# Kernel tuning notes

Hardware: AMD Instinct MI355X
Metric: run time of the kernel (lower is better)

Reference implementation:

```python
import jax, jax.numpy as jnp
import numpy as np

H = 1024      # hidden_dim
NH = 16       # num_heads
HD = H // NH  # head_dim
EPS = 1e-12
SCALE = float(np.sqrt(H))


def setup_inputs() -> dict:
    key = jax.random.key(0)
    ks = jax.random.split(key, 12)
    S, B = 2048, 2
    inp = {
        "query": jax.random.normal(ks[0], (S, B, 2 * H), jnp.float32),
        "key":   jax.random.normal(ks[1], (S, B, H), jnp.float32),
        "value": jax.random.normal(ks[2], (S, B, H), jnp.float32),
        # gating params (zeros in torch init, but randomize for a meaningful test)
        "qs": jax.random.normal(ks[3], (1, 1, H), jnp.float32) * 0.02,
        "ks_p": jax.random.normal(ks[4], (1, 1, H), jnp.float32) * 0.02,
        "vs": jax.random.normal(ks[5], (1, 1, H), jnp.float32) * 0.02,
        # Overparam vq: Linear(H, 2H)
        "vq_w": jax.random.normal(ks[6], (2 * H, H), jnp.float32) * (1.0 / np.sqrt(H)),
        "vq_b": jax.random.normal(ks[7], (2 * H,), jnp.float32) * 0.02,
        # q_linear: Linear(2H, H)
        "ql_w": jax.random.normal(ks[8], (H, 2 * H), jnp.float32) * (1.0 / np.sqrt(2 * H)),
        "ql_b": jax.random.normal(ks[9], (H,), jnp.float32) * 0.02,
        # LayerNorm(H)
        "ln_g": jnp.ones((H,), jnp.float32),
        "ln_b": jnp.zeros((H,), jnp.float32),
    }
    return inp


def _layernorm(x, g, b):
    mu = jnp.mean(x, axis=-1, keepdims=True)
    var = jnp.mean(jnp.square(x - mu), axis=-1, keepdims=True)
    return (x - mu) * jax.lax.rsqrt(var + EPS) * g + b


def reference(query, key, value, qs, ks_p, vs, vq_w, vq_b, ql_w, ql_b, ln_g, ln_b):
    # gate vectors
    qsig = jax.nn.sigmoid(qs)            # [1,1,H]
    ksig = jax.nn.sigmoid(ks_p)          # [1,1,H]
    # vq = Overparam(sigmoid(vs)): c,f = l1(x).split(H); sigmoid(f)*tanh(c)
    h = jax.nn.sigmoid(vs) @ vq_w.T + vq_b   # [1,1,2H]
    c, f = h[..., :H], h[..., H:]
    vsig = jax.nn.sigmoid(f) * jnp.tanh(c)   # [1,1,H]

    q = qsig * _layernorm(query @ ql_w.T + ql_b, ln_g, ln_b)  # [S,B,H]
    k = ksig * key
    v = vsig * value

    # batch-first
    q = jnp.transpose(q, (1, 0, 2))  # [B,Q,H]
    k = jnp.transpose(k, (1, 0, 2))  # [B,K,H]
    v = jnp.transpose(v, (1, 0, 2))
    B, Q, _ = q.shape
    K = k.shape[1]

    qh = q.reshape(B, Q, NH, HD)
    kh = k.reshape(B, K, NH, HD)
    vh = v.reshape(B, K, NH, HD)

    scores = jnp.einsum('bqhd,bkhd->bhqk', qh, kh) / SCALE
    w = jax.nn.softmax(scores, axis=-1)                # [B,NH,Q,K]
    out = jnp.einsum('bhqk,bkhd->bqhd', w, vh).reshape(B, Q, H)
    # torch code's final .transpose(0,1) is not assigned -> output is [Q,B,H]
    return jnp.transpose(out, (1, 0, 2))
```

## Files before the change

### kernel.cpp

```cpp
#include <hip/hip_runtime.h>

typedef __bf16 bf16x8 __attribute__((ext_vector_type(8)));
typedef float f32x4 __attribute__((ext_vector_type(4)));
typedef unsigned short u16x8 __attribute__((ext_vector_type(8)));
typedef unsigned short u16x4 __attribute__((ext_vector_type(4)));
typedef unsigned short u16;
typedef unsigned int u32;


#define LOG2E 1.4426950408889634f

__device__ __forceinline__ float b2f(u16 u) {
  union { unsigned int i; float f; } x; x.i = ((unsigned int)u) << 16; return x.f;
}
__device__ __forceinline__ u16 f2b(float f) {
  union { float f; unsigned int i; } x; x.f = f;
  unsigned int r = (x.i + 0x7fffu + ((x.i >> 16) & 1u)) >> 16;
  return (u16)r;
}
__device__ __forceinline__ float sigm(float x) { return 1.0f / (1.0f + __expf(-x)); }

__device__ __forceinline__ void async16(u16* lds, const u16* g) {
  __builtin_amdgcn_global_load_lds((const __attribute__((address_space(1))) void*)g,
                                   (__attribute__((address_space(3))) void*)lds, 16, 0, 0);
}

__global__ __launch_bounds__(256) void k_cvt_all(const float4* __restrict__ q, u16x4* __restrict__ qd,
                                                 const float4* __restrict__ w, u16x4* __restrict__ wd,
                                                 const float4* __restrict__ k, u16x4* __restrict__ kd,
                                                 const float4* __restrict__ v, u16x4* __restrict__ vd) {
  int b = blockIdx.x;
  const float4* s; u16x4* d; int i;
  if (b < 8192)       { s = q; d = qd; i = b * 256 + threadIdx.x; }
  else if (b < 10240) { s = w; d = wd; i = (b - 8192) * 256 + threadIdx.x; }
  else if (b < 14336) { s = k; d = kd; i = (b - 10240) * 256 + threadIdx.x; }
  else                { s = v; d = vd; i = (b - 14336) * 256 + threadIdx.x; }
  float4 x = s[i];
  u16x4 o; o[0] = f2b(x.x); o[1] = f2b(x.y); o[2] = f2b(x.z); o[3] = f2b(x.w);
  d[i] = o;
}

__global__ __launch_bounds__(256) void k_h(const float* __restrict__ vs,
                                           const float* __restrict__ vq_w,
                                           const float* __restrict__ vq_b,
                                           float* __restrict__ h) {
  __shared__ float svs[1024];
  int t = threadIdx.x;
  for (int i = t; i < 1024; i += 256) svs[i] = sigm(vs[i]);
  __syncthreads();
  int wave = t >> 6, lane = t & 63;
  int row = blockIdx.x * 4 + wave;
  const float4* w4 = (const float4*)(vq_w + (size_t)row * 1024);
  const float4* s4 = (const float4*)svs;
  float acc = 0.f;
#pragma unroll
  for (int k = 0; k < 4; ++k) {
    float4 w = w4[k * 64 + lane];
    float4 s = s4[k * 64 + lane];
    acc += w.x * s.x + w.y * s.y + w.z * s.z + w.w * s.w;
  }
#pragma unroll
  for (int off = 1; off < 64; off <<= 1) acc += __shfl_xor(acc, off);
  if (lane == 0) h[row] = acc + vq_b[row];
}

__global__ __launch_bounds__(256) void k_gemm(const u16* __restrict__ A,
                                              const u16* __restrict__ Bt,
                                              u16* __restrict__ C) {
  __shared__ __align__(16) u16 As[128 * 32];
  __shared__ __align__(16) u16 Bs[128 * 32];
  int tid = threadIdx.x;
  int wave = tid >> 6, lane = tid & 63;
  int l15 = lane & 15, quad = lane >> 4;
  int bx = blockIdx.x & 255;
  int kh = blockIdx.x >> 8;
  int kofs = kh << 10;
  int m0 = (bx >> 3) * 128;
  int n0 = (bx & 7) * 128;
  int wm = (wave >> 1) * 64, wn = (wave & 1) * 64;
  f32x4 acc[4][4] = {};
  int c1 = tid, c2 = tid + 256;
  const u16* ga1 = A + (size_t)(m0 + (c1 >> 2)) * 2048 + kofs + (c1 & 3) * 8;
  const u16* ga2 = A + (size_t)(m0 + (c2 >> 2)) * 2048 + kofs + (c2 & 3) * 8;
  const u16* gb1 = Bt + (size_t)(n0 + (c1 >> 2)) * 2048 + kofs + (c1 & 3) * 8;
  const u16* gb2 = Bt + (size_t)(n0 + (c2 >> 2)) * 2048 + kofs + (c2 & 3) * 8;
  u16* lA1 = As + wave * 512;
  u16* lA2 = As + 2048 + wave * 512;
  u16* lB1 = Bs + wave * 512;
  u16* lB2 = Bs + 2048 + wave * 512;
  for (int kt = 0; kt < 32; ++kt) {
    async16(lA1, ga1); async16(lA2, ga2);
    async16(lB1, gb1); async16(lB2, gb2);
    ga1 += 32; ga2 += 32; gb1 += 32; gb2 += 32;
    __syncthreads();
    bf16x8 af[4], bfr[4];
#pragma unroll
    for (int mt = 0; mt < 4; ++mt)
      af[mt] = *(const bf16x8*)(As + (wm + mt * 16 + l15) * 32 + quad * 8);
#pragma unroll
    for (int nt = 0; nt < 4; ++nt)
      bfr[nt] = *(const bf16x8*)(Bs + (wn + nt * 16 + l15) * 32 + quad * 8);
#pragma unroll
    for (int mt = 0; mt < 4; ++mt)
#pragma unroll
      for (int nt = 0; nt < 4; ++nt)
        acc[mt][nt] = __builtin_amdgcn_mfma_f32_16x16x32_bf16(af[mt], bfr[nt], acc[mt][nt], 0, 0, 0);
    __syncthreads();
  }
  u16* Cp = C + (size_t)kh * 4096 * 1024;
#pragma unroll
  for (int mt = 0; mt < 4; ++mt) {
#pragma unroll
    for (int r = 0; r < 4; ++r) {
      int m = m0 + wm + mt * 16 + quad * 4 + r;
      u16* crow = Cp + (size_t)m * 1024 + n0 + wn + l15;
#pragma unroll
      for (int nt = 0; nt < 4; ++nt) crow[nt * 16] = f2b(acc[mt][nt][r]);
    }
  }
}

__global__ __launch_bounds__(256) void k_ln(const u16* __restrict__ qpre0,
                                            const u16* __restrict__ qpre1,
                                            const float* __restrict__ ql_b,
                                            const float* __restrict__ ln_g,
                                            const float* __restrict__ ln_b,
                                            const float* __restrict__ qs,
                                            const float* __restrict__ ks,
                                            u16* __restrict__ qatt) {
  int row = blockIdx.x;
  int t = threadIdx.x;
  u16x4 a4 = *(const u16x4*)(qpre0 + (size_t)row * 1024 + t * 4);
  u16x4 b4 = *(const u16x4*)(qpre1 + (size_t)row * 1024 + t * 4);
  float v[4];
  float s = 0.f, ss = 0.f;
#pragma unroll
  for (int j = 0; j < 4; ++j) {
    v[j] = b2f(a4[j]) + b2f(b4[j]) + ql_b[t * 4 + j];
    s += v[j]; ss += v[j] * v[j];
  }
#pragma unroll
  for (int off = 1; off < 64; off <<= 1) { s += __shfl_xor(s, off); ss += __shfl_xor(ss, off); }
  __shared__ float red[8];
  int wv = t >> 6, ln = t & 63;
  if (ln == 0) { red[wv] = s; red[4 + wv] = ss; }
  __syncthreads();
  s = red[0] + red[1] + red[2] + red[3];
  ss = red[4] + red[5] + red[6] + red[7];
  float mu = s * (1.f / 1024.f);
  float rstd = rsqrtf(ss * (1.f / 1024.f) - mu * mu + 1e-12f);
  int sidx = row >> 1, b = row & 1;
  int ch0 = t * 4;
  int hh = ch0 >> 6, hd0 = ch0 & 63;
  u16* dst = qatt + ((size_t)(b * 16 + hh) * 2048 + sidx) * 64 + hd0;
#pragma unroll
  for (int j = 0; j < 4; ++j) {
    int ch = ch0 + j;
    float gate = sigm(qs[ch]) * sigm(ks[ch]) * (LOG2E / 32.0f);
    float y = (v[j] - mu) * rstd * ln_g[ch] + ln_b[ch];
    dst[j] = f2b(y * gate);
  }
}

__global__ __launch_bounds__(256, 2) void k_attn(const u16* __restrict__ qatt,
                                                 const u16* __restrict__ key,
                                                 const u16* __restrict__ value,
                                                 const float* __restrict__ hbuf,
                                                 float* __restrict__ out) {
  int bh = blockIdx.x & 31;
  int qt = blockIdx.x >> 5;
  int b = bh >> 4, h = bh & 15;
  int tid = threadIdx.x, wave = tid >> 6, lane = tid & 63;
  int l15 = lane & 15, quad = lane >> 4;
  int q0 = qt * 128;

  __shared__ __align__(16) u16 Kt[2][64 * 72];
  __shared__ __align__(16) u16 Vt[2][64 * 72];
  __shared__ __align__(16) u16 Pb[4][32 * 72];

  bf16x8 qf[2][2];
#pragma unroll
  for (int f = 0; f < 2; ++f) {
    const u16* qrow = qatt + ((size_t)bh * 2048 + q0 + f * 64 + wave * 16 + l15) * 64 + quad * 8;
    qf[f][0] = *(const bf16x8*)qrow;
    qf[f][1] = *(const bf16x8*)(qrow + 32);
  }

  const u16* kb = key + (size_t)b * 1024 + (size_t)h * 64;
  const u16* vb = value + (size_t)b * 1024 + (size_t)h * 64;
  u16* Pw = Pb[wave];

  int p = lane & 31;
  int chbase = wave * 16 + (lane >> 5) * 8;
  const u16* vsrc = vb + (size_t)2 * p * 2048 + chbase;
  int krow = wave * 16 + (lane >> 3);
  int kch  = (lane & 7) * 8;
  const u16* ksrc = kb + (size_t)krow * 2048 + kch;
  int kdofs = krow * 72 + kch;
  int vdofs_base = 2 * p;

  {
    u16x8 k0 = *(const u16x8*)ksrc;
    u16x8 k1 = *(const u16x8*)(ksrc + (size_t)8 * 2048);
    *(u16x8*)(&Kt[0][kdofs]) = k0;
    *(u16x8*)(&Kt[0][kdofs + 8 * 72]) = k1;
    u16x8 va = *(const u16x8*)vsrc;
    u16x8 vbq = *(const u16x8*)(vsrc + 2048);
#pragma unroll
    for (int c = 0; c < 8; ++c) {
      u32 pk = (u32)va[c] | ((u32)vbq[c] << 16);
      *(u32*)(&Vt[0][(chbase + c) * 72 + vdofs_base]) = pk;
    }
  }
  __syncthreads();

  f32x4 oacc[2][4] = {};
  float l_i[2][4] = {};

  for (int kt = 0; kt < 32; ++kt) {
    int cur = kt & 1;
    f32x4 sacc[2][4] = {};
    const u16* ktc = Kt[cur];
#pragma unroll
    for (int nt = 0; nt < 4; ++nt) {
      const u16* kr = ktc + (nt * 16 + l15) * 72 + quad * 8;
      bf16x8 kfa = *(const bf16x8*)kr;
      bf16x8 kfb = *(const bf16x8*)(kr + 32);
      sacc[0][nt] = __builtin_amdgcn_mfma_f32_16x16x32_bf16(qf[0][0], kfa, sacc[0][nt], 0, 0, 0);
      sacc[0][nt] = __builtin_amdgcn_mfma_f32_16x16x32_bf16(qf[0][1], kfb, sacc[0][nt], 0, 0, 0);
      sacc[1][nt] = __builtin_amdgcn_mfma_f32_16x16x32_bf16(qf[1][0], kfa, sacc[1][nt], 0, 0, 0);
      sacc[1][nt] = __builtin_amdgcn_mfma_f32_16x16x32_bf16(qf[1][1], kfb, sacc[1][nt], 0, 0, 0);
    }
    u16x8 pk0, pk1, va, vbq;
    if (kt < 31) {
      const u16* ks2 = ksrc + (size_t)(kt + 1) * 64 * 2048;
      pk0 = *(const u16x8*)ks2;
      pk1 = *(const u16x8*)(ks2 + (size_t)8 * 2048);
      const u16* vs2 = vsrc + (size_t)(kt + 1) * 64 * 2048;
      va = *(const u16x8*)vs2;
      vbq = *(const u16x8*)(vs2 + 2048);
    }
#pragma unroll
    for (int f = 0; f < 2; ++f) {
#pragma unroll
      for (int r = 0; r < 4; ++r) {
        float p0 = __builtin_amdgcn_exp2f(sacc[f][0][r]);
        float p1 = __builtin_amdgcn_exp2f(sacc[f][1][r]);
        float p2 = __builtin_amdgcn_exp2f(sacc[f][2][r]);
        float p3 = __builtin_amdgcn_exp2f(sacc[f][3][r]);
        l_i[f][r] += (p0 + p1) + (p2 + p3);
        u16* prow = Pw + (f * 16 + quad * 4 + r) * 72 + l15;
        prow[0]  = f2b(p0);
        prow[16] = f2b(p1);
        prow[32] = f2b(p2);
        prow[48] = f2b(p3);
      }
    }
    bf16x8 pf[2][2];
#pragma unroll
    for (int f = 0; f < 2; ++f) {
      pf[f][0] = *(const bf16x8*)(Pw + (f * 16 + l15) * 72 + quad * 8);
      pf[f][1] = *(const bf16x8*)(Pw + (f * 16 + l15) * 72 + 32 + quad * 8);
    }
    const u16* vt = Vt[cur];
#pragma unroll
    for (int nt = 0; nt < 4; ++nt) {
      const u16* vr = vt + (nt * 16 + l15) * 72 + quad * 8;
      bf16x8 vf0 = *(const bf16x8*)vr;
      bf16x8 vf1 = *(const bf16x8*)(vr + 32);
      oacc[0][nt] = __builtin_amdgcn_mfma_f32_16x16x32_bf16(pf[0][0], vf0, oacc[0][nt], 0, 0, 0);
      oacc[0][nt] = __builtin_amdgcn_mfma_f32_16x16x32_bf16(pf[0][1], vf1, oacc[0][nt], 0, 0, 0);
      oacc[1][nt] = __builtin_amdgcn_mfma_f32_16x16x32_bf16(pf[1][0], vf0, oacc[1][nt], 0, 0, 0);
      oacc[1][nt] = __builtin_amdgcn_mfma_f32_16x16x32_bf16(pf[1][1], vf1, oacc[1][nt], 0, 0, 0);
    }
    if (kt < 31) {
      u16* kd = Kt[cur ^ 1];
      *(u16x8*)(&kd[kdofs]) = pk0;
      *(u16x8*)(&kd[kdofs + 8 * 72]) = pk1;
      u16* vd = Vt[cur ^ 1];
#pragma unroll
      for (int c = 0; c < 8; ++c) {
        u32 pk = (u32)va[c] | ((u32)vbq[c] << 16);
        *(u32*)(&vd[(chbase + c) * 72 + vdofs_base]) = pk;
      }
    }
    __syncthreads();
  }
#pragma unroll
  for (int f = 0; f < 2; ++f)
#pragma unroll
    for (int r = 0; r < 4; ++r) {
      float l = l_i[f][r];
      l += __shfl_xor(l, 1);
      l += __shfl_xor(l, 2);
      l += __shfl_xor(l, 4);
      l += __shfl_xor(l, 8);
      l_i[f][r] = l;
    }
  float vsg[4];
#pragma unroll
  for (int nt = 0; nt < 4; ++nt) {
    int ch = h * 64 + nt * 16 + l15;
    vsg[nt] = sigm(hbuf[1024 + ch]) * tanhf(hbuf[ch]);
  }
#pragma unroll
  for (int f = 0; f < 2; ++f)
#pragma unroll
    for (int r = 0; r < 4; ++r) {
      int sq = q0 + f * 64 + wave * 16 + quad * 4 + r;
      float inv = 1.0f / l_i[f][r];
      float* orow = out + ((size_t)sq * 2 + b) * 1024 + h * 64;
#pragma unroll
      for (int nt = 0; nt < 4; ++nt)
        orow[nt * 16 + l15] = oacc[f][nt][r] * inv * vsg[nt];
    }
}

extern "C" void kernel_launch(void* const* d_in, const int* in_sizes, int n_in,
                              void* d_out, int out_size, void* d_ws, size_t ws_size,
                              hipStream_t stream) {
  (void)in_sizes; (void)n_in; (void)out_size; (void)ws_size;
  const float* query = (const float*)d_in[0];
  const float* key   = (const float*)d_in[1];
  const float* value = (const float*)d_in[2];
  const float* qs    = (const float*)d_in[3];
  const float* ksp   = (const float*)d_in[4];
  const float* vs    = (const float*)d_in[5];
  const float* vq_w  = (const float*)d_in[6];
  const float* vq_b  = (const float*)d_in[7];
  const float* ql_w  = (const float*)d_in[8];
  const float* ql_b  = (const float*)d_in[9];
  const float* ln_g  = (const float*)d_in[10];
  const float* ln_b  = (const float*)d_in[11];
  float* out = (float*)d_out;

  float* ws = (float*)d_ws;
  float* h   = ws;
  u16* qpre  = (u16*)(ws + 4096);
  u16* qbf   = qpre + (size_t)2 * 4096 * 1024;
  u16* qatt  = qbf;
  u16* wbf   = qbf + (size_t)4096 * 2048;
  u16* kbf   = wbf + (size_t)1024 * 2048;
  u16* vbf   = kbf + (size_t)4096 * 1024;

  hipLaunchKernelGGL(k_cvt_all, dim3(18432), dim3(256), 0, stream,
                     (const float4*)query, (u16x4*)qbf,
                     (const float4*)ql_w,  (u16x4*)wbf,
                     (const float4*)key,   (u16x4*)kbf,
                     (const float4*)value, (u16x4*)vbf);
  hipLaunchKernelGGL(k_h,    dim3(512),  dim3(256), 0, stream, vs, vq_w, vq_b, h);
  hipLaunchKernelGGL(k_gemm, dim3(512),  dim3(256), 0, stream, qbf, wbf, qpre);
  hipLaunchKernelGGL(k_ln,   dim3(4096), dim3(256), 0, stream, qpre, qpre + (size_t)4096 * 1024,
                     ql_b, ln_g, ln_b, qs, ksp, qatt);
  hipLaunchKernelGGL(k_attn, dim3(512),  dim3(256), 0, stream, qatt, kbf, vbf, h, out);
}
```

Before: 242.8 us.

## Fuse K/V bf16 conversion into attention loads and split GEMM K four ways

Key and value are no longer converted to bf16 by a separate pass. The attention kernel now reads fp32 K/V directly and converts them to bf16 while staging into LDS, which removes a write and re-read of about 16MB of bf16 data. The GEMM split-K goes from 2 to 4 partitions (1024 blocks), and the layernorm kernel sums four partial bf16 outputs. The costs are doubled global read bytes inside the attention kernel, extra conversion work on its critical path, and more partial-sum traffic and bf16 rounding error in the GEMM.

```diff
diff --git a/kernel.cpp b/kernel.cpp
--- a/kernel.cpp
+++ b/kernel.cpp
@@ -24,17 +24,19 @@
   __builtin_amdgcn_global_load_lds((const __attribute__((address_space(1))) void*)g,
                                    (__attribute__((address_space(3))) void*)lds, 16, 0, 0);
 }
-
-__global__ __launch_bounds__(256) void k_cvt_all(const float4* __restrict__ q, u16x4* __restrict__ qd,
-                                                 const float4* __restrict__ w, u16x4* __restrict__ wd,
-                                                 const float4* __restrict__ k, u16x4* __restrict__ kd,
-                                                 const float4* __restrict__ v, u16x4* __restrict__ vd) {
+__device__ __forceinline__ u16x8 cvt8(f32x4 a, f32x4 b) {
+  u16x8 o;
+  o[0] = f2b(a[0]); o[1] = f2b(a[1]); o[2] = f2b(a[2]); o[3] = f2b(a[3]);
+  o[4] = f2b(b[0]); o[5] = f2b(b[1]); o[6] = f2b(b[2]); o[7] = f2b(b[3]);
+  return o;
+}
+
+__global__ __launch_bounds__(256) void k_cvt2(const float4* __restrict__ q, u16x4* __restrict__ qd,
+                                              const float4* __restrict__ w, u16x4* __restrict__ wd) {
   int b = blockIdx.x;
   const float4* s; u16x4* d; int i;
-  if (b < 8192)       { s = q; d = qd; i = b * 256 + threadIdx.x; }
-  else if (b < 10240) { s = w; d = wd; i = (b - 8192) * 256 + threadIdx.x; }
-  else if (b < 14336) { s = k; d = kd; i = (b - 10240) * 256 + threadIdx.x; }
-  else                { s = v; d = vd; i = (b - 14336) * 256 + threadIdx.x; }
+  if (b < 8192) { s = q; d = qd; i = b * 256 + threadIdx.x; }
+  else          { s = w; d = wd; i = (b - 8192) * 256 + threadIdx.x; }
   float4 x = s[i];
   u16x4 o; o[0] = f2b(x.x); o[1] = f2b(x.y); o[2] = f2b(x.z); o[3] = f2b(x.w);
   d[i] = o;
@@ -74,7 +76,7 @@
   int l15 = lane & 15, quad = lane >> 4;
   int bx = blockIdx.x & 255;
   int kh = blockIdx.x >> 8;
-  int kofs = kh << 10;
+  int kofs = kh << 9;
   int m0 = (bx >> 3) * 128;
   int n0 = (bx & 7) * 128;
   int wm = (wave >> 1) * 64, wn = (wave & 1) * 64;
@@ -88,7 +90,7 @@
   u16* lA2 = As + 2048 + wave * 512;
   u16* lB1 = Bs + wave * 512;
   u16* lB2 = Bs + 2048 + wave * 512;
-  for (int kt = 0; kt < 32; ++kt) {
+  for (int kt = 0; kt < 16; ++kt) {
     async16(lA1, ga1); async16(lA2, ga2);
     async16(lB1, gb1); async16(lB2, gb2);
     ga1 += 32; ga2 += 32; gb1 += 32; gb2 += 32;
@@ -120,8 +122,7 @@
   }
 }
 
-__global__ __launch_bounds__(256) void k_ln(const u16* __restrict__ qpre0,
-                                            const u16* __restrict__ qpre1,
+__global__ __launch_bounds__(256) void k_ln(const u16* __restrict__ qpre,
                                             const float* __restrict__ ql_b,
                                             const float* __restrict__ ln_g,
                                             const float* __restrict__ ln_b,
@@ -130,13 +131,16 @@
                                             u16* __restrict__ qatt) {
   int row = blockIdx.x;
   int t = threadIdx.x;
-  u16x4 a4 = *(const u16x4*)(qpre0 + (size_t)row * 1024 + t * 4);
-  u16x4 b4 = *(const u16x4*)(qpre1 + (size_t)row * 1024 + t * 4);
+  const u16* base = qpre + (size_t)row * 1024 + t * 4;
+  u16x4 p0 = *(const u16x4*)(base);
+  u16x4 p1 = *(const u16x4*)(base + (size_t)4096 * 1024);
+  u16x4 p2 = *(const u16x4*)(base + (size_t)2 * 4096 * 1024);
+  u16x4 p3 = *(const u16x4*)(base + (size_t)3 * 4096 * 1024);
   float v[4];
   float s = 0.f, ss = 0.f;
 #pragma unroll
   for (int j = 0; j < 4; ++j) {
-    v[j] = b2f(a4[j]) + b2f(b4[j]) + ql_b[t * 4 + j];
+    v[j] = ((b2f(p0[j]) + b2f(p1[j])) + (b2f(p2[j]) + b2f(p3[j]))) + ql_b[t * 4 + j];
     s += v[j]; ss += v[j] * v[j];
   }
 #pragma unroll
@@ -163,8 +167,8 @@
 }
 
 __global__ __launch_bounds__(256, 2) void k_attn(const u16* __restrict__ qatt,
-                                                 const u16* __restrict__ key,
-                                                 const u16* __restrict__ value,
+                                                 const float* __restrict__ key,
+                                                 const float* __restrict__ value,
                                                  const float* __restrict__ hbuf,
                                                  float* __restrict__ out) {
   int bh = blockIdx.x & 31;
@@ -186,30 +190,36 @@
     qf[f][1] = *(const bf16x8*)(qrow + 32);
   }
 
-  const u16* kb = key + (size_t)b * 1024 + (size_t)h * 64;
-  const u16* vb = value + (size_t)b * 1024 + (size_t)h * 64;
+  const float* kb = key + (size_t)b * 1024 + (size_t)h * 64;
+  const float* vb = value + (size_t)b * 1024 + (size_t)h * 64;
   u16* Pw = Pb[wave];
 
   int p = lane & 31;
   int chbase = wave * 16 + (lane >> 5) * 8;
-  const u16* vsrc = vb + (size_t)2 * p * 2048 + chbase;
+  const float* vsrc = vb + (size_t)2 * p * 2048 + chbase;
   int krow = wave * 16 + (lane >> 3);
   int kch  = (lane & 7) * 8;
-  const u16* ksrc = kb + (size_t)krow * 2048 + kch;
+  const float* ksrc = kb + (size_t)krow * 2048 + kch;
   int kdofs = krow * 72 + kch;
   int vdofs_base = 2 * p;
 
   {
-    u16x8 k0 = *(const u16x8*)ksrc;
-    u16x8 k1 = *(const u16x8*)(ksrc + (size_t)8 * 2048);
-    *(u16x8*)(&Kt[0][kdofs]) = k0;
-    *(u16x8*)(&Kt[0][kdofs + 8 * 72]) = k1;
-    u16x8 va = *(const u16x8*)vsrc;
-    u16x8 vbq = *(const u16x8*)(vsrc + 2048);
-#pragma unroll
-    for (int c = 0; c < 8; ++c) {
-      u32 pk = (u32)va[c] | ((u32)vbq[c] << 16);
+    f32x4 ka0 = *(const f32x4*)ksrc;
+    f32x4 ka1 = *(const f32x4*)(ksrc + 4);
+    f32x4 kb0 = *(const f32x4*)(ksrc + (size_t)8 * 2048);
+    f32x4 kb1 = *(const f32x4*)(ksrc + (size_t)8 * 2048 + 4);
+    *(u16x8*)(&Kt[0][kdofs]) = cvt8(ka0, ka1);
+    *(u16x8*)(&Kt[0][kdofs + 8 * 72]) = cvt8(kb0, kb1);
+    f32x4 v0a = *(const f32x4*)vsrc;
+    f32x4 v0b = *(const f32x4*)(vsrc + 4);
+    f32x4 v1a = *(const f32x4*)(vsrc + 2048);
+    f32x4 v1b = *(const f32x4*)(vsrc + 2048 + 4);
+#pragma unroll
+    for (int c = 0; c < 4; ++c) {
+      u32 pk = (u32)f2b(v0a[c]) | ((u32)f2b(v1a[c]) << 16);
       *(u32*)(&Vt[0][(chbase + c) * 72 + vdofs_base]) = pk;
+      u32 pk2 = (u32)f2b(v0b[c]) | ((u32)f2b(v1b[c]) << 16);
+      *(u32*)(&Vt[0][(chbase + 4 + c) * 72 + vdofs_base]) = pk2;
     }
   }
   __syncthreads();
@@ -231,14 +241,18 @@
       sacc[1][nt] = __builtin_amdgcn_mfma_f32_16x16x32_bf16(qf[1][0], kfa, sacc[1][nt], 0, 0, 0);
       sacc[1][nt] = __builtin_amdgcn_mfma_f32_16x16x32_bf16(qf[1][1], kfb, sacc[1][nt], 0, 0, 0);
     }
-    u16x8 pk0, pk1, va, vbq;
+    f32x4 ka0, ka1, kb0, kb1, v0a, v0b, v1a, v1b;
     if (kt < 31) {
-      const u16* ks2 = ksrc + (size_t)(kt + 1) * 64 * 2048;
-      pk0 = *(const u16x8*)ks2;
-      pk1 = *(const u16x8*)(ks2 + (size_t)8 * 2048);
-      const u16* vs2 = vsrc + (size_t)(kt + 1) * 64 * 2048;
-      va = *(const u16x8*)vs2;
-      vbq = *(const u16x8*)(vs2 + 2048);
+      const float* ks2 = ksrc + (size_t)(kt + 1) * 64 * 2048;
+      ka0 = *(const f32x4*)ks2;
+      ka1 = *(const f32x4*)(ks2 + 4);
+      kb0 = *(const f32x4*)(ks2 + (size_t)8 * 2048);
+      kb1 = *(const f32x4*)(ks2 + (size_t)8 * 2048 + 4);
+      const float* vs2 = vsrc + (size_t)(kt + 1) * 64 * 2048;
+      v0a = *(const f32x4*)vs2;
+      v0b = *(const f32x4*)(vs2 + 4);
+      v1a = *(const f32x4*)(vs2 + 2048);
+      v1b = *(const f32x4*)(vs2 + 2048 + 4);
     }
 #pragma unroll
     for (int f = 0; f < 2; ++f) {
@@ -275,13 +289,15 @@
     }
     if (kt < 31) {
       u16* kd = Kt[cur ^ 1];
-      *(u16x8*)(&kd[kdofs]) = pk0;
-      *(u16x8*)(&kd[kdofs + 8 * 72]) = pk1;
+      *(u16x8*)(&kd[kdofs]) = cvt8(ka0, ka1);
+      *(u16x8*)(&kd[kdofs + 8 * 72]) = cvt8(kb0, kb1);
       u16* vd = Vt[cur ^ 1];
 #pragma unroll
-      for (int c = 0; c < 8; ++c) {
-        u32 pk = (u32)va[c] | ((u32)vbq[c] << 16);
+      for (int c = 0; c < 4; ++c) {
+        u32 pk = (u32)f2b(v0a[c]) | ((u32)f2b(v1a[c]) << 16);
         *(u32*)(&vd[(chbase + c) * 72 + vdofs_base]) = pk;
+        u32 pk2 = (u32)f2b(v0b[c]) | ((u32)f2b(v1b[c]) << 16);
+        *(u32*)(&vd[(chbase + 4 + c) * 72 + vdofs_base]) = pk2;
       }
     }
     __syncthreads();
@@ -337,20 +353,16 @@
   float* ws = (float*)d_ws;
   float* h   = ws;
   u16* qpre  = (u16*)(ws + 4096);
-  u16* qbf   = qpre + (size_t)2 * 4096 * 1024;
+  u16* qbf   = qpre + (size_t)4 * 4096 * 1024;
   u16* qatt  = qbf;
   u16* wbf   = qbf + (size_t)4096 * 2048;
-  u16* kbf   = wbf + (size_t)1024 * 2048;
-  u16* vbf   = kbf + (size_t)4096 * 1024;
-
-  hipLaunchKernelGGL(k_cvt_all, dim3(18432), dim3(256), 0, stream,
+
+  hipLaunchKernelGGL(k_cvt2, dim3(10240), dim3(256), 0, stream,
                      (const float4*)query, (u16x4*)qbf,
-                     (const float4*)ql_w,  (u16x4*)wbf,
-                     (const float4*)key,   (u16x4*)kbf,
-                     (const float4*)value, (u16x4*)vbf);
+                     (const float4*)ql_w,  (u16x4*)wbf);
   hipLaunchKernelGGL(k_h,    dim3(512),  dim3(256), 0, stream, vs, vq_w, vq_b, h);
-  hipLaunchKernelGGL(k_gemm, dim3(512),  dim3(256), 0, stream, qbf, wbf, qpre);
-  hipLaunchKernelGGL(k_ln,   dim3(4096), dim3(256), 0, stream, qpre, qpre + (size_t)4096 * 1024,
+  hipLaunchKernelGGL(k_gemm, dim3(1024), dim3(256), 0, stream, qbf, wbf, qpre);
+  hipLaunchKernelGGL(k_ln,   dim3(4096), dim3(256), 0, stream, qpre,
                      ql_b, ln_g, ln_b, qs, ksp, qatt);
-  hipLaunchKernelGGL(k_attn, dim3(512),  dim3(256), 0, stream, qatt, kbf, vbf, h, out);
-}
+  hipLaunchKernelGGL(k_attn, dim3(512),  dim3(256), 0, stream, qatt, key, value, h, out);
+}
```

Measured after the change: 243.5 us. No clear change (+0.3%).
